# Optimization experiments

Hardware: AMD Instinct MI355X
Metric: run time of the kernel (lower is better)

The kernel has to match this reference:

```python
import math
import jax, jax.numpy as jnp
from jax import lax
import numpy as np

N = 512          # transform size; frame size = 2N
B = 16           # batch
T = 2048         # number of frames; signal length = N*T
PI = math.pi


def _make_mdct_filter(n: int, normalize: bool = True) -> jnp.ndarray:
    # filter[k, 0, t] = cos(pi/N * (t + 0.5 + N/2) * (k + 0.5)) / sqrt(N)
    k = jnp.arange(n, dtype=jnp.float32).reshape(n, 1, 1)
    t = jnp.arange(2 * n, dtype=jnp.float32).reshape(1, 1, 2 * n)
    f = jnp.cos(PI / n * (t + 0.5 + n / 2) * (k + 0.5))
    if normalize:
        f = f / jnp.sqrt(jnp.float32(n))
    return f  # [N, 1, 2N]


def setup_inputs() -> dict:
    key = jax.random.key(0)
    x = jax.random.normal(key, (B, 1, N * T), dtype=jnp.float32)
    mdct_filter = _make_mdct_filter(N, normalize=True)
    return {"x": x, "mdct_filter": mdct_filter}


def reference(x, mdct_filter):
    # Equivalent of F.conv1d(x, filter, stride=N, padding=N)
    n = mdct_filter.shape[0]
    # x: [B, 1, N*T] -> out: [B, N, T+1]
    out = lax.conv_general_dilated(
        x, mdct_filter,
        window_strides=(n,),
        padding=[(n, n)],
        dimension_numbers=("NCH", "OIH", "NCH"),
    )
    return out
```

## Files before the change

### kernel.cpp

```cpp
#include <hip/hip_runtime.h>
#include <hip/hip_bf16.h>
#include <stdint.h>
#include <stddef.h>


constexpr int N_ = 512;
constexpr int T_ = 2048;
constexpr int B_ = 16;
constexpr int LEN = N_ * T_;
constexpr int FRAMES = T_ + 1;
constexpr int COLS = B_ * FRAMES;
constexpr int NT_TILES = 257;
constexpr int COLS_PAD = NT_TILES * 128;
constexpr int KF = 512;
constexpr int BK = 64;

typedef __attribute__((ext_vector_type(8))) _Float16 f16x8;
typedef __attribute__((ext_vector_type(4))) _Float16 f16x4;
typedef __attribute__((ext_vector_type(4))) float f32x4;

#define GLD16(gptr, lptr)                                                     \
  __builtin_amdgcn_global_load_lds(                                           \
      (const __attribute__((address_space(1))) unsigned int*)(gptr),          \
      (__attribute__((address_space(3))) unsigned int*)(lptr), 16, 0, 0)

__global__ void prep_filter(const float* __restrict__ f,
                            _Float16* __restrict__ D) {
  int idx = (blockIdx.x * 256 + threadIdx.x) * 4;
  int k = idx >> 9;
  int j = idx & 511;
  int t = (j < 256) ? j : (j + 256);
  const float4 v = *(const float4*)&f[k * 1024 + t];
  f16x4 h = {(_Float16)v.x, (_Float16)v.y, (_Float16)v.z, (_Float16)v.w};
  *(f16x4*)&D[k * KF + j] = h;
}

__global__ void fold_x(const float* __restrict__ x, _Float16* __restrict__ V) {
  const int half = threadIdx.x >> 7;
  const int t = threadIdx.x & 127;
  const int c = blockIdx.x * 2 + half;
  int jbase;
  float4 va = {0.f, 0.f, 0.f, 0.f}, vb = {0.f, 0.f, 0.f, 0.f};
  float s;
  if (t < 64) { jbase = t * 4; s = -1.0f; }
  else        { jbase = 256 + (t - 64) * 4; s = 1.0f; }
  if (c < COLS) {
    int b = c / FRAMES;
    int o = c - b * FRAMES;
    const float* xb = x + (size_t)b * LEN;
    int g = o * N_ - N_;
    int i0, i1r;
    if (t < 64) { i0 = g + jbase;       i1r = g + 508 - jbase; }
    else        { int u = t - 64; i0 = g + 512 + u * 4; i1r = g + 1020 - u * 4; }
    if ((unsigned)i0 <= (unsigned)(LEN - 4))  va = *(const float4*)&xb[i0];
    if ((unsigned)i1r <= (unsigned)(LEN - 4)) vb = *(const float4*)&xb[i1r];
  }
  f16x4 h;
  h[0] = (_Float16)(va.x + s * vb.w);
  h[1] = (_Float16)(va.y + s * vb.z);
  h[2] = (_Float16)(va.z + s * vb.y);
  h[3] = (_Float16)(va.w + s * vb.x);
  *(f16x4*)&V[(size_t)c * KF + jbase] = h;
}

__global__ __launch_bounds__(256, 4) void gemm_fold(
    const _Float16* __restrict__ D, const _Float16* __restrict__ V,
    float* __restrict__ out) {
  __shared__ __align__(16) _Float16 As[128 * BK];
  __shared__ __align__(16) _Float16 Bs[128 * BK];

  const int m0 = blockIdx.x * 128;
  const int n0 = blockIdx.y * 128;
  const int tid = threadIdx.x;
  const int wid = tid >> 6;
  const int lane = tid & 63;
  const int quad = lane >> 4;
  const int l16 = lane & 15;
  const int mw = (wid >> 1) * 64;
  const int nw = (wid & 1) * 64;

  f32x4 acc[4][4];
#pragma unroll
  for (int i = 0; i < 4; ++i)
#pragma unroll
    for (int j = 0; j < 4; ++j) acc[i][j] = (f32x4){0.f, 0.f, 0.f, 0.f};

  for (int kt = 0; kt < KF / BK; ++kt) {
    const int kb = kt * BK;
    __syncthreads();
#pragma unroll
    for (int it = 0; it < 4; ++it) {
      const int S = it * 256 + tid;
      const int r = S >> 3;
      const int c = (S & 7) ^ (r & 7);
      const int goff = kb + c * 8;
      GLD16(D + (size_t)(m0 + r) * KF + goff, &As[S * 8]);
      GLD16(V + (size_t)(n0 + r) * KF + goff, &Bs[S * 8]);
    }
    __syncthreads();

#pragma unroll
    for (int ko = 0; ko < 2; ++ko) {
      f16x8 af[4], bf[4];
#pragma unroll
      for (int i = 0; i < 4; ++i) {
        int ra = mw + i * 16 + l16;
        int rb = nw + i * 16 + l16;
        int ca = ko * 4 + quad;
        af[i] = *(const f16x8*)&As[(ra * 8 + (ca ^ (ra & 7))) * 8];
        bf[i] = *(const f16x8*)&Bs[(rb * 8 + (ca ^ (rb & 7))) * 8];
      }
#pragma unroll
      for (int i = 0; i < 4; ++i)
#pragma unroll
        for (int j = 0; j < 4; ++j)
          acc[i][j] = __builtin_amdgcn_mfma_f32_16x16x32_f16(af[i], bf[j], acc[i][j], 0, 0, 0);
    }
  }

#pragma unroll
  for (int i = 0; i < 4; ++i) {
#pragma unroll
    for (int j = 0; j < 4; ++j) {
      int col = n0 + nw + j * 16 + l16;
      if (col < COLS) {
        int b = col / FRAMES;
        int o = col - b * FRAMES;
        int rowb = m0 + mw + i * 16 + quad * 4;
        float* op = out + (size_t)b * N_ * FRAMES + (size_t)rowb * FRAMES + o;
#pragma unroll
        for (int r = 0; r < 4; ++r) op[(size_t)r * FRAMES] = acc[i][j][r];
      }
    }
  }
}

__global__ void naive_conv(const float* __restrict__ x, const float* __restrict__ f,
                           float* __restrict__ out) {
  int col = blockIdx.x;
  int k = threadIdx.x;
  __shared__ float win[1024];
  int b = col / FRAMES;
  int o = col - b * FRAMES;
  const float* xb = x + (size_t)b * LEN;
  int g = o * N_ - N_;
  for (int t = threadIdx.x; t < 1024; t += 512) {
    int i = g + t;
    win[t] = (i >= 0 && i < LEN) ? xb[i] : 0.0f;
  }
  __syncthreads();
  float s = 0.0f;
  const float* fk = f + (size_t)k * 1024;
  for (int t = 0; t < 1024; ++t) s += win[t] * fk[t];
  out[(size_t)b * N_ * FRAMES + (size_t)k * FRAMES + o] = s;
}

extern "C" void kernel_launch(void* const* d_in, const int* in_sizes, int n_in,
                              void* d_out, int out_size, void* d_ws, size_t ws_size,
                              hipStream_t stream) {
  const float* x = (const float*)d_in[0];
  const float* f = (const float*)d_in[1];
  float* out = (float*)d_out;

  const size_t elems_D = (size_t)512 * 512;
  const size_t elems_V = (size_t)COLS_PAD * KF;
  const size_t need = (elems_D + elems_V) * sizeof(_Float16);

  if (ws_size < need) {
    naive_conv<<<COLS, 512, 0, stream>>>(x, f, out);
    return;
  }

  _Float16* D = (_Float16*)d_ws;
  _Float16* V = D + elems_D;

  prep_filter<<<256, 256, 0, stream>>>(f, D);
  fold_x<<<COLS_PAD / 2, 256, 0, stream>>>(x, V);
  gemm_fold<<<dim3(4, NT_TILES), 256, 0, stream>>>(D, V, out);
}
```

Measured before the change: 148.7 us.

## Fuse MDCT input folding into GEMM B-tile load, drop intermediate buffer

Removes the separate fold_x kernel and its fp16 V workspace. The GEMM now loads raw fp32 input windows, applies the symmetric fold with a sign, converts to fp16, and writes the B tile into swizzled shared memory. This removes a kernel launch and a write-then-read of the large intermediate buffer. In exchange, each of the four M-blocks repeats the fold work and reads fp32 input through registers instead of async global-to-LDS loads, and launch bounds drop occupancy from 4 to 3 blocks.

New measurement: 186.7 us. 1.26x slower.

```diff
diff --git a/kernel.cpp b/kernel.cpp
--- a/kernel.cpp
+++ b/kernel.cpp
@@ -11,7 +11,6 @@
 constexpr int FRAMES = T_ + 1;
 constexpr int COLS = B_ * FRAMES;
 constexpr int NT_TILES = 257;
-constexpr int COLS_PAD = NT_TILES * 128;
 constexpr int KF = 512;
 constexpr int BK = 64;
 
@@ -35,36 +34,8 @@
   *(f16x4*)&D[k * KF + j] = h;
 }
 
-__global__ void fold_x(const float* __restrict__ x, _Float16* __restrict__ V) {
-  const int half = threadIdx.x >> 7;
-  const int t = threadIdx.x & 127;
-  const int c = blockIdx.x * 2 + half;
-  int jbase;
-  float4 va = {0.f, 0.f, 0.f, 0.f}, vb = {0.f, 0.f, 0.f, 0.f};
-  float s;
-  if (t < 64) { jbase = t * 4; s = -1.0f; }
-  else        { jbase = 256 + (t - 64) * 4; s = 1.0f; }
-  if (c < COLS) {
-    int b = c / FRAMES;
-    int o = c - b * FRAMES;
-    const float* xb = x + (size_t)b * LEN;
-    int g = o * N_ - N_;
-    int i0, i1r;
-    if (t < 64) { i0 = g + jbase;       i1r = g + 508 - jbase; }
-    else        { int u = t - 64; i0 = g + 512 + u * 4; i1r = g + 1020 - u * 4; }
-    if ((unsigned)i0 <= (unsigned)(LEN - 4))  va = *(const float4*)&xb[i0];
-    if ((unsigned)i1r <= (unsigned)(LEN - 4)) vb = *(const float4*)&xb[i1r];
-  }
-  f16x4 h;
-  h[0] = (_Float16)(va.x + s * vb.w);
-  h[1] = (_Float16)(va.y + s * vb.z);
-  h[2] = (_Float16)(va.z + s * vb.y);
-  h[3] = (_Float16)(va.w + s * vb.x);
-  *(f16x4*)&V[(size_t)c * KF + jbase] = h;
-}
-
-__global__ __launch_bounds__(256, 4) void gemm_fold(
-    const _Float16* __restrict__ D, const _Float16* __restrict__ V,
+__global__ __launch_bounds__(256, 3) void gemm_fused(
+    const _Float16* __restrict__ D, const float* __restrict__ x,
     float* __restrict__ out) {
   __shared__ __align__(16) _Float16 As[128 * BK];
   __shared__ __align__(16) _Float16 Bs[128 * BK];
@@ -79,23 +50,74 @@
   const int mw = (wid >> 1) * 64;
   const int nw = (wid & 1) * 64;
 
+  const int rbase = tid >> 3;
+  const int cch = tid & 7;
+  const int swz = cch ^ (rbase & 7);
+  int gg[4], lo[4];
+  bool ok[4];
+#pragma unroll
+  for (int u = 0; u < 4; ++u) {
+    int r = u * 32 + rbase;
+    int col = n0 + r;
+    int b = (int)((unsigned)col / (unsigned)FRAMES);
+    int o = col - b * FRAMES;
+    gg[u] = b * LEN + o * N_ - N_;
+    lo[u] = b * LEN;
+    ok[u] = (col < COLS);
+  }
+
   f32x4 acc[4][4];
 #pragma unroll
   for (int i = 0; i < 4; ++i)
 #pragma unroll
     for (int j = 0; j < 4; ++j) acc[i][j] = (f32x4){0.f, 0.f, 0.f, 0.f};
 
+  const _Float16* Dm = D + (size_t)m0 * KF;
+
   for (int kt = 0; kt < KF / BK; ++kt) {
     const int kb = kt * BK;
     __syncthreads();
+
 #pragma unroll
-    for (int it = 0; it < 4; ++it) {
-      const int S = it * 256 + tid;
-      const int r = S >> 3;
-      const int c = (S & 7) ^ (r & 7);
-      const int goff = kb + c * 8;
-      GLD16(D + (size_t)(m0 + r) * KF + goff, &As[S * 8]);
-      GLD16(V + (size_t)(n0 + r) * KF + goff, &Bs[S * 8]);
+    for (int u = 0; u < 4; ++u) {
+      const int S = u * 256 + tid;
+      const int rA = S >> 3;
+      const int cA = (S & 7) ^ (rA & 7);
+      GLD16(Dm + (size_t)rA * KF + kb + cA * 8, &As[S * 8]);
+    }
+
+    const int j0 = kb + cch * 8;
+    const bool mi = (kb < 256);
+    const int fo = mi ? j0 : (j0 + 256);
+    const int ro = mi ? (504 - j0) : (1272 - j0);
+    const float sgn = mi ? -1.0f : 1.0f;
+#pragma unroll
+    for (int u = 0; u < 4; ++u) {
+      float4 a0 = {0.f, 0.f, 0.f, 0.f}, a1 = {0.f, 0.f, 0.f, 0.f};
+      float4 r0 = {0.f, 0.f, 0.f, 0.f}, r1 = {0.f, 0.f, 0.f, 0.f};
+      if (ok[u]) {
+        const int fb = gg[u] + fo;
+        const int rb = gg[u] + ro;
+        if ((unsigned)(fb - lo[u]) <= (unsigned)(LEN - 8)) {
+          a0 = *(const float4*)(x + fb);
+          a1 = *(const float4*)(x + fb + 4);
+        }
+        if ((unsigned)(rb - lo[u]) <= (unsigned)(LEN - 8)) {
+          r0 = *(const float4*)(x + rb);
+          r1 = *(const float4*)(x + rb + 4);
+        }
+      }
+      f16x8 h;
+      h[0] = (_Float16)__builtin_fmaf(sgn, r1.w, a0.x);
+      h[1] = (_Float16)__builtin_fmaf(sgn, r1.z, a0.y);
+      h[2] = (_Float16)__builtin_fmaf(sgn, r1.y, a0.z);
+      h[3] = (_Float16)__builtin_fmaf(sgn, r1.x, a0.w);
+      h[4] = (_Float16)__builtin_fmaf(sgn, r0.w, a1.x);
+      h[5] = (_Float16)__builtin_fmaf(sgn, r0.z, a1.y);
+      h[6] = (_Float16)__builtin_fmaf(sgn, r0.y, a1.z);
+      h[7] = (_Float16)__builtin_fmaf(sgn, r0.x, a1.w);
+      const int r = u * 32 + rbase;
+      *(f16x8*)&Bs[(r * 8 + swz) * 8] = h;
     }
     __syncthreads();
 
@@ -162,19 +184,13 @@
   const float* f = (const float*)d_in[1];
   float* out = (float*)d_out;
 
-  const size_t elems_D = (size_t)512 * 512;
-  const size_t elems_V = (size_t)COLS_PAD * KF;
-  const size_t need = (elems_D + elems_V) * sizeof(_Float16);
-
+  const size_t need = (size_t)512 * 512 * sizeof(_Float16);
   if (ws_size < need) {
     naive_conv<<<COLS, 512, 0, stream>>>(x, f, out);
     return;
   }
 
   _Float16* D = (_Float16*)d_ws;
-  _Float16* V = D + elems_D;
-
   prep_filter<<<256, 256, 0, stream>>>(f, D);
-  fold_x<<<COLS_PAD / 2, 256, 0, stream>>>(x, V);
-  gemm_fold<<<dim3(4, NT_TILES), 256, 0, stream>>>(D, V, out);
+  gemm_fused<<<dim3(4, NT_TILES), 256, 0, stream>>>(D, x, out);
 }
```
